# Optimization experiments

Hardware: AMD Instinct MI355X
Metric: run time of the kernel (lower is better)

The kernel has to match this reference:

```python
import jax, jax.numpy as jnp
import numpy as np

B, T, C = 2, 2048, 2048
NH, NKVH = 16, 4
HS = C // NH  # 128
NEG_INF = -1e30


def _rope_freqs(T, hs, base=10000.0):
    inv = 1.0 / (base ** (np.arange(0, hs, 2, dtype=np.float32) / hs))  # [hs/2]
    ang = np.arange(T, dtype=np.float32)[:, None] * inv[None, :]        # [T, hs/2]
    return jnp.asarray(np.cos(ang)), jnp.asarray(np.sin(ang))


def setup_inputs() -> dict:
    key = jax.random.key(0)
    ks = jax.random.split(key, 4)
    x = jax.random.normal(ks[0], (B, T, C), dtype=jnp.float32)
    W_attn = jax.random.normal(ks[1], (C, C + 2 * NKVH * HS), dtype=jnp.float32) * 0.02
    b_attn = jnp.zeros((C + 2 * NKVH * HS,), dtype=jnp.float32)
    W_proj = jax.random.normal(ks[2], (C, C), dtype=jnp.float32) * 0.02
    b_proj = jnp.zeros((C,), dtype=jnp.float32)
    freqs_cos, freqs_sin = _rope_freqs(T, HS)
    return {"x": x, "freqs_cos": freqs_cos, "freqs_sin": freqs_sin,
            "W_attn": W_attn, "b_attn": b_attn, "W_proj": W_proj, "b_proj": b_proj}


def _apply_rope(x, cos, sin):
    # x: [B, T, H, hs]; cos/sin: [T, hs/2] -> broadcast [1, T, 1, hs/2]
    b, t, h, hs = x.shape
    x_ = x.reshape(b, t, h, hs // 2, 2)
    re, im = x_[..., 0], x_[..., 1]
    c = cos[None, :, None, :]
    s = sin[None, :, None, :]
    out_re = re * c - im * s
    out_im = re * s + im * c
    return jnp.stack([out_re, out_im], axis=-1).reshape(b, t, h, hs)


def reference(x, freqs_cos, freqs_sin, W_attn, b_attn, W_proj, b_proj):
    b, t, c = x.shape
    qkv = x @ W_attn + b_attn                                   # [B,T,C+2*nkvh*hs]
    q, k, v = jnp.split(qkv, [c, c + NKVH * HS], axis=2)
    q = q.reshape(b, t, NH, HS)
    k = k.reshape(b, t, NKVH, HS)
    v = v.reshape(b, t, NKVH, HS)
    q = _apply_rope(q, freqs_cos, freqs_sin)
    k = _apply_rope(k, freqs_cos, freqs_sin)
    # group heads: q [B, nkvh, rep, T, hs]; k,v [B, nkvh, T, hs]
    rep = NH // NKVH
    q = q.transpose(0, 2, 1, 3).reshape(b, NKVH, rep, t, HS)
    k = k.transpose(0, 2, 1, 3)
    v = v.transpose(0, 2, 1, 3)
    scale = 1.0 / jnp.sqrt(jnp.asarray(HS, dtype=x.dtype))
    scores = jnp.einsum('bgrth,bgsh->bgrts', q, k) * scale      # [B,g,rep,T,T]
    causal = jnp.tril(jnp.ones((t, t), dtype=bool))
    scores = jnp.where(causal[None, None, None], scores, NEG_INF)
    att = jax.nn.softmax(scores, axis=-1)
    y = jnp.einsum('bgrts,bgsh->bgrth', att, v)                 # [B,g,rep,T,hs]
    y = y.reshape(b, NH, t, HS).transpose(0, 2, 1, 3).reshape(b, t, c)
    return y @ W_proj + b_proj
```

## Files before the change

kernel.cpp:

```cpp
#include <hip/hip_runtime.h>
#include <hip/hip_bf16.h>
#include <stdint.h>

#define B_ 2
#define T_ 2048
#define C_ 2048
#define NH_ 16
#define NKVH_ 4
#define HS_ 128
#define QKV_ 3072
#define NTOK_ 4096

typedef __attribute__((ext_vector_type(4))) float f32x4;
typedef __attribute__((ext_vector_type(8))) short s16x8;

__device__ __forceinline__ short f2bf(float f) {
    union { float f; unsigned u; } v; v.f = f;
    unsigned r = v.u + 0x7FFFu + ((v.u >> 16) & 1u);
    return (short)(r >> 16);
}

__device__ __forceinline__ void async16(const void* g, void* l) {
    __builtin_amdgcn_global_load_lds(
        (const __attribute__((address_space(1))) void*)g,
        (__attribute__((address_space(3))) void*)l, 16, 0, 0);
}

__global__ void cast_bf16_kernel(const float* __restrict__ x, short* __restrict__ out, int n8) {
    int i = blockIdx.x * 256 + threadIdx.x;
    if (i >= n8) return;
    const float4* p = (const float4*)x + (size_t)i * 2;
    float4 a = p[0], b = p[1];
    short o[8] = { f2bf(a.x), f2bf(a.y), f2bf(a.z), f2bf(a.w),
                   f2bf(b.x), f2bf(b.y), f2bf(b.z), f2bf(b.w) };
    *(int4*)(out + (size_t)i * 8) = *(const int4*)o;
}

__global__ void transcast(const float* __restrict__ W, short* __restrict__ WT, int Kd, int Nd) {
    __shared__ float tile[64][65];
    int k0 = blockIdx.x * 64, n0 = blockIdx.y * 64;
    int tid = threadIdx.x;
    int cl = tid & 63, rw = tid >> 6;
    for (int it = 0; it < 16; ++it) {
        int r = it * 4 + rw;
        tile[r][cl] = W[(size_t)(k0 + r) * Nd + n0 + cl];
    }
    __syncthreads();
    for (int it = 0; it < 16; ++it) {
        int n = it * 4 + rw;
        WT[(size_t)(n0 + n) * Kd + k0 + cl] = f2bf(tile[cl][n]);
    }
}

__global__ __launch_bounds__(256, 2) void gemm_bt(
    const short* __restrict__ A, const short* __restrict__ Bt,
    const float* __restrict__ bias, float* __restrict__ Cc,
    int M, int N, int K)
{
    __shared__ short As[128 * 64];
    __shared__ short Bs[128 * 64];
    int tid = threadIdx.x;
    int w = tid >> 6, l = tid & 63;
    int lr = l & 15, lg = l >> 4;
    int bm = blockIdx.x, bn = blockIdx.y;
    int wm = (w >> 1) * 64, wn = (w & 1) * 64;
    f32x4 acc[4][4];
#pragma unroll
    for (int i = 0; i < 4; i++)
#pragma unroll
        for (int j = 0; j < 4; j++) { acc[i][j][0]=0.f; acc[i][j][1]=0.f; acc[i][j][2]=0.f; acc[i][j][3]=0.f; }
    int arow = l >> 3, acol = (l & 7) * 8;
    for (int k0 = 0; k0 < K; k0 += 64) {
#pragma unroll
        for (int i = 0; i < 4; i++) {
            int chunk = w * 4 + i;
            int row = chunk * 8 + arow;
            async16(A  + (size_t)(bm * 128 + row) * K + k0 + acol, (char*)As + chunk * 1024);
            async16(Bt + (size_t)(bn * 128 + row) * K + k0 + acol, (char*)Bs + chunk * 1024);
        }
        __syncthreads();
#pragma unroll
        for (int ks = 0; ks < 2; ks++) {
            s16x8 af[4], bf[4];
#pragma unroll
            for (int mi = 0; mi < 4; mi++)
                af[mi] = *(const s16x8*)&As[(wm + mi * 16 + lr) * 64 + ks * 32 + lg * 8];
#pragma unroll
            for (int ni = 0; ni < 4; ni++)
                bf[ni] = *(const s16x8*)&Bs[(wn + ni * 16 + lr) * 64 + ks * 32 + lg * 8];
#pragma unroll
            for (int mi = 0; mi < 4; mi++)
#pragma unroll
                for (int ni = 0; ni < 4; ni++)
                    acc[mi][ni] = __builtin_amdgcn_mfma_f32_16x16x32_bf16(af[mi], bf[ni], acc[mi][ni], 0, 0, 0);
        }
        __syncthreads();
    }
#pragma unroll
    for (int mi = 0; mi < 4; mi++) {
        int row = bm * 128 + wm + mi * 16 + lg * 4;
#pragma unroll
        for (int ni = 0; ni < 4; ni++) {
            int col = bn * 128 + wn + ni * 16 + lr;
            float bv = bias[col];
#pragma unroll
            for (int j = 0; j < 4; j++)
                Cc[(size_t)(row + j) * N + col] = acc[mi][ni][j] + bv;
        }
    }
}

__global__ void rope_scatter(const float* __restrict__ qkv,
                             const float* __restrict__ fcos, const float* __restrict__ fsin,
                             short* __restrict__ Q, short* __restrict__ Kb)
{
    int idx = blockIdx.x * 256 + threadIdx.x;
    int tok = idx / 1280, p = idx - tok * 1280;
    if (tok >= NTOK_) return;
    int b = tok >> 11, t = tok & 2047;
    if (p < 1024) {
        int h = p >> 6, i = p & 63;
        const float* src = qkv + (size_t)tok * QKV_ + h * 128 + 2 * i;
        float re = src[0], im = src[1];
        float c = fcos[t * 64 + i], s = fsin[t * 64 + i];
        unsigned lo = (unsigned short)f2bf(re * c - im * s);
        unsigned hi = (unsigned short)f2bf(re * s + im * c);
        *(unsigned*)(Q + ((size_t)(b * NH_ + h) * T_ + t) * HS_ + 2 * i) = lo | (hi << 16);
    } else {
        int pk = p - 1024; int g = pk >> 6, i = pk & 63;
        const float* src = qkv + (size_t)tok * QKV_ + C_ + g * 128 + 2 * i;
        float re = src[0], im = src[1];
        float c = fcos[t * 64 + i], s = fsin[t * 64 + i];
        unsigned lo = (unsigned short)f2bf(re * c - im * s);
        unsigned hi = (unsigned short)f2bf(re * s + im * c);
        *(unsigned*)(Kb + ((size_t)(b * NKVH_ + g) * T_ + t) * HS_ + 2 * i) = lo | (hi << 16);
    }
}

__global__ void v_transpose(const float* __restrict__ qkv, short* __restrict__ VT) {
    __shared__ float tile[64][65];
    int t0 = blockIdx.x * 64, d0 = blockIdx.y * 64;
    int bg = blockIdx.z; int b = bg >> 2, g = bg & 3;
    int tid = threadIdx.x; int cl = tid & 63, rw = tid >> 6;
    const float* base = qkv + (size_t)(b * T_ + t0) * QKV_ + C_ + NKVH_ * HS_ + g * HS_ + d0;
    for (int it = 0; it < 16; ++it) {
        int r = it * 4 + rw;
        tile[r][cl] = base[(size_t)r * QKV_ + cl];
    }
    __syncthreads();
    short* out = VT + ((size_t)(b * NKVH_ + g) * HS_ + d0) * T_ + t0;
    for (int it = 0; it < 16; ++it) {
        int d = it * 4 + rw;
        out[(size_t)d * T_ + cl] = f2bf(tile[cl][d]);
    }
}

__global__ __launch_bounds__(256, 2) void attn_kernel(
    const short* __restrict__ Qg, const short* __restrict__ Kg,
    const short* __restrict__ VTg, short* __restrict__ Y)
{
    __shared__ short Ks[64 * 128];
    __shared__ short VTs[128 * 64];
    __shared__ short Ps[4][16 * 64];
    int tid = threadIdx.x, w = tid >> 6, l = tid & 63;
    int lr = l & 15, lg = l >> 4;
    int qt = 31 - (int)blockIdx.y;
    int bh = blockIdx.x;
    int b = bh >> 4, h = bh & 15, g = h >> 2;
    const short* Qb = Qg + (size_t)(b * NH_ + h) * T_ * HS_;
    const short* Kb = Kg + (size_t)(b * NKVH_ + g) * T_ * HS_;
    const short* Vb = VTg + (size_t)(b * NKVH_ + g) * HS_ * T_;

    s16x8 qf[4];
    int qrow = qt * 64 + w * 16 + lr;
#pragma unroll
    for (int kc = 0; kc < 4; kc++)
        qf[kc] = *(const s16x8*)(Qb + (size_t)qrow * HS_ + kc * 32 + lg * 8);

    f32x4 oacc[8];
#pragma unroll
    for (int i = 0; i < 8; i++) { oacc[i][0]=0.f; oacc[i][1]=0.f; oacc[i][2]=0.f; oacc[i][3]=0.f; }
    float m[4] = {-1e30f, -1e30f, -1e30f, -1e30f};
    float lsum[4] = {0.f, 0.f, 0.f, 0.f};
    const float scale = 0.08838834764831845f;
    int qg0 = qt * 64 + w * 16 + lg * 4;

    for (int st = 0; st <= qt; ++st) {
#pragma unroll
        for (int i = 0; i < 4; i++) {
            int chunk = w * 4 + i;
            int poff = chunk * 1024 + l * 16;
            int qoffk = poff ^ (((poff >> 8) & 7) << 4);
            async16(Kb + (size_t)(st * 64 + (qoffk >> 8)) * HS_ + ((qoffk & 255) >> 1),
                    (char*)Ks + chunk * 1024);
            int qoffv = poff ^ (((poff >> 7) & 7) << 4);
            async16(Vb + (size_t)(qoffv >> 7) * T_ + st * 64 + ((qoffv & 127) >> 1),
                    (char*)VTs + chunk * 1024);
        }
        __syncthreads();

        f32x4 sv[4];
#pragma unroll
        for (int ni = 0; ni < 4; ni++) {
            f32x4 a; a[0]=0.f; a[1]=0.f; a[2]=0.f; a[3]=0.f;
#pragma unroll
            for (int kc = 0; kc < 4; kc++) {
                int lo = ((ni * 16 + lr) << 8) + ((kc * 32 + lg * 8) << 1);
                int po = lo ^ (((lo >> 8) & 7) << 4);
                s16x8 kf = *(const s16x8*)((const char*)Ks + po);
                a = __builtin_amdgcn_mfma_f32_16x16x32_bf16(qf[kc], kf, a, 0, 0, 0);
            }
            sv[ni] = a;
        }
        float tmax[4] = {-1e30f, -1e30f, -1e30f, -1e30f};
#pragma unroll
        for (int ni = 0; ni < 4; ni++) {
            int sg = st * 64 + ni * 16 + lr;
#pragma unroll
            for (int j = 0; j < 4; j++) {
                float s = sv[ni][j] * scale;
                if (sg > qg0 + j) s = -1e30f;
                sv[ni][j] = s;
                tmax[j] = fmaxf(tmax[j], s);
            }
        }
#pragma unroll
        for (int msk = 1; msk < 16; msk <<= 1)
#pragma unroll
            for (int j = 0; j < 4; j++)
                tmax[j] = fmaxf(tmax[j], __shfl_xor(tmax[j], msk));
        float corr[4];
#pragma unroll
        for (int j = 0; j < 4; j++) {
            float mn = fmaxf(m[j], tmax[j]);
            corr[j] = __expf(m[j] - mn);
            m[j] = mn;
        }
        float rsum[4] = {0.f, 0.f, 0.f, 0.f};
#pragma unroll
        for (int ni = 0; ni < 4; ni++)
#pragma unroll
            for (int j = 0; j < 4; j++) {
                float p = __expf(sv[ni][j] - m[j]);
                sv[ni][j] = p;
                rsum[j] += p;
            }
#pragma unroll
        for (int msk = 1; msk < 16; msk <<= 1)
#pragma unroll
            for (int j = 0; j < 4; j++)
                rsum[j] += __shfl_xor(rsum[j], msk);
#pragma unroll
        for (int j = 0; j < 4; j++)
            lsum[j] = lsum[j] * corr[j] + rsum[j];
#pragma unroll
        for (int dn = 0; dn < 8; dn++)
#pragma unroll
            for (int j = 0; j < 4; j++)
                oacc[dn][j] *= corr[j];
#pragma unroll
        for (int ni = 0; ni < 4; ni++)
#pragma unroll
            for (int j = 0; j < 4; j++) {
                int lo = (lg * 4 + j) * 128 + (ni * 16 + lr) * 2;
                int po = lo ^ (((lo >> 7) & 7) << 4);
                *(short*)((char*)&Ps[w][0] + po) = f2bf(sv[ni][j]);
            }
#pragma unroll
        for (int sc = 0; sc < 2; sc++) {
            int lo = lr * 128 + sc * 64 + lg * 16;
            int po = lo ^ (((lo >> 7) & 7) << 4);
            s16x8 pf = *(const s16x8*)((const char*)&Ps[w][0] + po);
#pragma unroll
            for (int dn = 0; dn < 8; dn++) {
                int lov = (dn * 16 + lr) * 128 + (sc * 32 + lg * 8) * 2;
                int pov = lov ^ (((lov >> 7) & 7) << 4);
                s16x8 vf = *(const s16x8*)((const char*)VTs + pov);
                oacc[dn] = __builtin_amdgcn_mfma_f32_16x16x32_bf16(pf, vf, oacc[dn], 0, 0, 0);
            }
        }
        __syncthreads();
    }

    float inv[4];
#pragma unroll
    for (int j = 0; j < 4; j++) inv[j] = 1.0f / lsum[j];
#pragma unroll
    for (int dn = 0; dn < 8; dn++)
#pragma unroll
        for (int j = 0; j < 4; j++) {
            int trow = qt * 64 + w * 16 + lg * 4 + j;
            Y[(size_t)(b * T_ + trow) * C_ + h * 128 + dn * 16 + lr] = f2bf(oacc[dn][j] * inv[j]);
        }
}

extern "C" void kernel_launch(void* const* d_in, const int* in_sizes, int n_in,
                              void* d_out, int out_size, void* d_ws, size_t ws_size,
                              hipStream_t stream)
{
    const float* x      = (const float*)d_in[0];
    const float* fcos   = (const float*)d_in[1];
    const float* fsin   = (const float*)d_in[2];
    const float* W_attn = (const float*)d_in[3];
    const float* b_attn = (const float*)d_in[4];
    const float* W_proj = (const float*)d_in[5];
    const float* b_proj = (const float*)d_in[6];
    float* out = (float*)d_out;
    char* ws = (char*)d_ws;

    short* xb  = (short*)(ws + 0);
    float* qkv = (float*)(ws + 16777216);
    short* y   = (short*)(ws + 16777216);
    short* WpT = (short*)(ws + 33554432);
    short* WaT = (short*)(ws + 67108864);
    short* Qb  = (short*)(ws + 67108864);
    short* Kb  = (short*)(ws + 83886080);
    short* VT  = (short*)(ws + 88080384);

    cast_bf16_kernel<<<4096, 256, 0, stream>>>(x, xb, NTOK_ * C_ / 8);
    transcast<<<dim3(32, 48), 256, 0, stream>>>(W_attn, WaT, C_, QKV_);
    gemm_bt<<<dim3(32, 24), 256, 0, stream>>>(xb, WaT, b_attn, qkv, NTOK_, QKV_, C_);
    rope_scatter<<<20480, 256, 0, stream>>>(qkv, fcos, fsin, Qb, Kb);
    v_transpose<<<dim3(32, 2, 8), 256, 0, stream>>>(qkv, VT);
    transcast<<<dim3(32, 32), 256, 0, stream>>>(W_proj, WpT, C_, C_);
    attn_kernel<<<dim3(32, 32), 256, 0, stream>>>(Qb, Kb, VT, y);
    gemm_bt<<<dim3(32, 16), 256, 0, stream>>>(y, WpT, b_proj, out, NTOK_, C_, C_);
}
```

Baseline: 244.4 us.

## Double-buffer K/V tiles and trim softmax work in attention kernel

Double-buffers the K and V^T shared-memory tiles so the async load of the next tile overlaps compute on the current one. The softmax scale is folded into Q during the RoPE step, and the causal mask now runs only on the diagonal tile. Output rescaling is skipped when no row max increases, and the per-row sum reduction is deferred to a single shuffle after the loop. In exchange LDS use doubles, which may limit occupancy at 2 blocks per CU, and rounding changes slightly because the scale is applied before bf16 conversion.

```diff
diff --git a/kernel.cpp b/kernel.cpp
--- a/kernel.cpp
+++ b/kernel.cpp
@@ -114,6 +114,7 @@
                              const float* __restrict__ fcos, const float* __restrict__ fsin,
                              short* __restrict__ Q, short* __restrict__ Kb)
 {
+    const float qscale = 0.08838834764831845f;
     int idx = blockIdx.x * 256 + threadIdx.x;
     int tok = idx / 1280, p = idx - tok * 1280;
     if (tok >= NTOK_) return;
@@ -123,8 +124,8 @@
         const float* src = qkv + (size_t)tok * QKV_ + h * 128 + 2 * i;
         float re = src[0], im = src[1];
         float c = fcos[t * 64 + i], s = fsin[t * 64 + i];
-        unsigned lo = (unsigned short)f2bf(re * c - im * s);
-        unsigned hi = (unsigned short)f2bf(re * s + im * c);
+        unsigned lo = (unsigned short)f2bf((re * c - im * s) * qscale);
+        unsigned hi = (unsigned short)f2bf((re * s + im * c) * qscale);
         *(unsigned*)(Q + ((size_t)(b * NH_ + h) * T_ + t) * HS_ + 2 * i) = lo | (hi << 16);
     } else {
         int pk = p - 1024; int g = pk >> 6, i = pk & 63;
@@ -159,8 +160,8 @@
     const short* __restrict__ Qg, const short* __restrict__ Kg,
     const short* __restrict__ VTg, short* __restrict__ Y)
 {
-    __shared__ short Ks[64 * 128];
-    __shared__ short VTs[128 * 64];
+    __shared__ short Ks[2][64 * 128];
+    __shared__ short VTs[2][128 * 64];
     __shared__ short Ps[4][16 * 64];
     int tid = threadIdx.x, w = tid >> 6, l = tid & 63;
     int lr = l & 15, lg = l >> 4;
@@ -171,33 +172,41 @@
     const short* Kb = Kg + (size_t)(b * NKVH_ + g) * T_ * HS_;
     const short* Vb = VTg + (size_t)(b * NKVH_ + g) * HS_ * T_;
 
-    s16x8 qf[4];
-    int qrow = qt * 64 + w * 16 + lr;
-#pragma unroll
-    for (int kc = 0; kc < 4; kc++)
-        qf[kc] = *(const s16x8*)(Qb + (size_t)qrow * HS_ + kc * 32 + lg * 8);
-
-    f32x4 oacc[8];
-#pragma unroll
-    for (int i = 0; i < 8; i++) { oacc[i][0]=0.f; oacc[i][1]=0.f; oacc[i][2]=0.f; oacc[i][3]=0.f; }
-    float m[4] = {-1e30f, -1e30f, -1e30f, -1e30f};
-    float lsum[4] = {0.f, 0.f, 0.f, 0.f};
-    const float scale = 0.08838834764831845f;
-    int qg0 = qt * 64 + w * 16 + lg * 4;
-
-    for (int st = 0; st <= qt; ++st) {
+    auto STAGE = [&](int st, int buf) {
 #pragma unroll
         for (int i = 0; i < 4; i++) {
             int chunk = w * 4 + i;
             int poff = chunk * 1024 + l * 16;
             int qoffk = poff ^ (((poff >> 8) & 7) << 4);
             async16(Kb + (size_t)(st * 64 + (qoffk >> 8)) * HS_ + ((qoffk & 255) >> 1),
-                    (char*)Ks + chunk * 1024);
+                    (char*)&Ks[buf][0] + chunk * 1024);
             int qoffv = poff ^ (((poff >> 7) & 7) << 4);
             async16(Vb + (size_t)(qoffv >> 7) * T_ + st * 64 + ((qoffv & 127) >> 1),
-                    (char*)VTs + chunk * 1024);
-        }
-        __syncthreads();
+                    (char*)&VTs[buf][0] + chunk * 1024);
+        }
+    };
+
+    s16x8 qf[4];
+    int qrow = qt * 64 + w * 16 + lr;
+#pragma unroll
+    for (int kc = 0; kc < 4; kc++)
+        qf[kc] = *(const s16x8*)(Qb + (size_t)qrow * HS_ + kc * 32 + lg * 8);
+
+    f32x4 oacc[8];
+#pragma unroll
+    for (int i = 0; i < 8; i++) { oacc[i][0]=0.f; oacc[i][1]=0.f; oacc[i][2]=0.f; oacc[i][3]=0.f; }
+    float m[4] = {-1e30f, -1e30f, -1e30f, -1e30f};
+    float lsum[4] = {0.f, 0.f, 0.f, 0.f};
+    int qg0 = qt * 64 + w * 16 + lg * 4;
+
+    STAGE(0, 0);
+    __syncthreads();
+    int cur = 0;
+
+    for (int st = 0; st <= qt; ++st) {
+        if (st < qt) STAGE(st + 1, cur ^ 1);
+        const char* KsC = (const char*)&Ks[cur][0];
+        const char* VsC = (const char*)&VTs[cur][0];
 
         f32x4 sv[4];
 #pragma unroll
@@ -207,57 +216,56 @@
             for (int kc = 0; kc < 4; kc++) {
                 int lo = ((ni * 16 + lr) << 8) + ((kc * 32 + lg * 8) << 1);
                 int po = lo ^ (((lo >> 8) & 7) << 4);
-                s16x8 kf = *(const s16x8*)((const char*)Ks + po);
+                s16x8 kf = *(const s16x8*)(KsC + po);
                 a = __builtin_amdgcn_mfma_f32_16x16x32_bf16(qf[kc], kf, a, 0, 0, 0);
             }
             sv[ni] = a;
         }
         float tmax[4] = {-1e30f, -1e30f, -1e30f, -1e30f};
-#pragma unroll
-        for (int ni = 0; ni < 4; ni++) {
-            int sg = st * 64 + ni * 16 + lr;
-#pragma unroll
-            for (int j = 0; j < 4; j++) {
-                float s = sv[ni][j] * scale;
-                if (sg > qg0 + j) s = -1e30f;
-                sv[ni][j] = s;
-                tmax[j] = fmaxf(tmax[j], s);
-            }
+        if (st == qt) {
+#pragma unroll
+            for (int ni = 0; ni < 4; ni++) {
+                int sg = st * 64 + ni * 16 + lr;
+#pragma unroll
+                for (int j = 0; j < 4; j++) {
+                    float s = sv[ni][j];
+                    if (sg > qg0 + j) s = -1e30f;
+                    sv[ni][j] = s;
+                    tmax[j] = fmaxf(tmax[j], s);
+                }
+            }
+        } else {
+#pragma unroll
+            for (int ni = 0; ni < 4; ni++)
+#pragma unroll
+                for (int j = 0; j < 4; j++)
+                    tmax[j] = fmaxf(tmax[j], sv[ni][j]);
         }
 #pragma unroll
         for (int msk = 1; msk < 16; msk <<= 1)
 #pragma unroll
             for (int j = 0; j < 4; j++)
                 tmax[j] = fmaxf(tmax[j], __shfl_xor(tmax[j], msk));
-        float corr[4];
-#pragma unroll
-        for (int j = 0; j < 4; j++) {
-            float mn = fmaxf(m[j], tmax[j]);
-            corr[j] = __expf(m[j] - mn);
-            m[j] = mn;
-        }
-        float rsum[4] = {0.f, 0.f, 0.f, 0.f};
+        bool need = (tmax[0] > m[0]) | (tmax[1] > m[1]) | (tmax[2] > m[2]) | (tmax[3] > m[3]);
+        if (__any(need)) {
+#pragma unroll
+            for (int j = 0; j < 4; j++) {
+                float mn = fmaxf(m[j], tmax[j]);
+                float corr = __expf(m[j] - mn);
+                m[j] = mn;
+                lsum[j] *= corr;
+#pragma unroll
+                for (int dn = 0; dn < 8; dn++) oacc[dn][j] *= corr;
+            }
+        }
 #pragma unroll
         for (int ni = 0; ni < 4; ni++)
 #pragma unroll
             for (int j = 0; j < 4; j++) {
                 float p = __expf(sv[ni][j] - m[j]);
                 sv[ni][j] = p;
-                rsum[j] += p;
-            }
-#pragma unroll
-        for (int msk = 1; msk < 16; msk <<= 1)
-#pragma unroll
-            for (int j = 0; j < 4; j++)
-                rsum[j] += __shfl_xor(rsum[j], msk);
-#pragma unroll
-        for (int j = 0; j < 4; j++)
-            lsum[j] = lsum[j] * corr[j] + rsum[j];
-#pragma unroll
-        for (int dn = 0; dn < 8; dn++)
-#pragma unroll
-            for (int j = 0; j < 4; j++)
-                oacc[dn][j] *= corr[j];
+                lsum[j] += p;
+            }
 #pragma unroll
         for (int ni = 0; ni < 4; ni++)
 #pragma unroll
@@ -275,13 +283,19 @@
             for (int dn = 0; dn < 8; dn++) {
                 int lov = (dn * 16 + lr) * 128 + (sc * 32 + lg * 8) * 2;
                 int pov = lov ^ (((lov >> 7) & 7) << 4);
-                s16x8 vf = *(const s16x8*)((const char*)VTs + pov);
+                s16x8 vf = *(const s16x8*)(VsC + pov);
                 oacc[dn] = __builtin_amdgcn_mfma_f32_16x16x32_bf16(pf, vf, oacc[dn], 0, 0, 0);
             }
         }
         __syncthreads();
-    }
-
+        cur ^= 1;
+    }
+
+#pragma unroll
+    for (int msk = 1; msk < 16; msk <<= 1)
+#pragma unroll
+        for (int j = 0; j < 4; j++)
+            lsum[j] += __shfl_xor(lsum[j], msk);
     float inv[4];
 #pragma unroll
     for (int j = 0; j < 4; j++) inv[j] = 1.0f / lsum[j];
```

Result: faster. 230.5 us (-5.7%).
